# Performance work log

Measured on AMD Instinct MI355X. Metric: run time of the kernel, lower is better.

Reference implementation:

```python
import jax, jax.numpy as jnp
import numpy as np

D_IN, D_MODEL = 512, 256
B, N = 2, 512


def setup_inputs() -> dict:
    key = jax.random.key(0)
    ks = jax.random.split(key, 8)
    xav_x = float(np.sqrt(2.0 / (D_IN + D_MODEL)))
    xav_p = float(np.sqrt(2.0 / (4 + D_MODEL)))
    return {
        "x": jax.random.normal(ks[0], (B, N, D_IN), dtype=jnp.float32),
        "pos": jax.random.normal(ks[1], (B, N, 4), dtype=jnp.float32),
        "attn_mask": jax.random.randint(ks[2], (B, N, N), 0, 2, dtype=jnp.int32),
        "Wx": jax.random.normal(ks[3], (D_IN, D_MODEL), dtype=jnp.float32) * xav_x,
        "bx": jnp.zeros((D_MODEL,), dtype=jnp.float32),
        "Wp": jax.random.normal(ks[4], (4, D_MODEL), dtype=jnp.float32) * xav_p,
        "bp": jnp.zeros((D_MODEL,), dtype=jnp.float32),
        "w": jax.random.normal(ks[5], (D_MODEL,), dtype=jnp.float32) * 0.05,
    }


def reference(x, pos, attn_mask, Wx, bx, Wp, bp, w):
    # projected, activated inputs: [B, N, d_model]
    h = jnp.tanh(x @ Wx + bx)
    # pairwise relative positions: [B, N, N, 4]
    rel = pos[:, :, None, :] - pos[:, None, :, :]
    # position MLP + tanh: [B, N, N, d_model]
    z = jnp.tanh(rel @ Wp + bp)
    # scores via dot with weight vector: [B, N, N]
    attn = jnp.einsum("bijd,d->bij", z, w)
    mask = attn_mask != 0
    attn = jnp.where(mask, attn, -jnp.inf)
    attn = jax.nn.softmax(attn, axis=2)
    attn = jnp.where(mask, attn, 0.0)
    # dropout is identity in eval mode
    # weighted sum: [B, N, d_model]
    output = jnp.einsum("bij,bjd->bid", attn, h)
    return (output, attn)
```

## Files before the change

### kernel.cpp

```cpp
#include <hip/hip_runtime.h>
#include <hip/hip_bf16.h>
#include <math.h>

#define BATCH   2
#define SEQ     512
#define DIN     512
#define DM      256
#define DM4     (DM/4)

#define LOG2E2  2.88539008177792681f

#if __has_builtin(__builtin_amdgcn_exp2f)
#define EXP2(x) __builtin_amdgcn_exp2f(x)
#else
#define EXP2(x) exp2f(x)
#endif
#if __has_builtin(__builtin_amdgcn_rcpf)
#define RCP(x) __builtin_amdgcn_rcpf(x)
#else
#define RCP(x) (1.0f / (x))
#endif

__device__ __forceinline__ float tanh_from_scaled(float targ) {
    return fmaf(-2.0f, RCP(1.0f + EXP2(targ)), 1.0f);
}

__global__ __launch_bounds__(512) void produce_k(
    const float* __restrict__ pos,
    const float* __restrict__ Wp,
    const float* __restrict__ x,
    const float* __restrict__ Wx,
    const float* __restrict__ bx,
    float4* __restrict__ EB4,
    float* __restrict__ h)
{
    const int tid = threadIdx.x;
    const int idx = blockIdx.x;

    if (idx < 128) {
        const int b  = idx >> 6;
        const int d4 = idx & 63;
        const int d0 = 4 * d4;
        const float4 p = ((const float4*)pos)[b * SEQ + tid];
        float4 e;
        {
            const float P = fmaf(p.x, Wp[d0], fmaf(p.y, Wp[DM + d0],
                            fmaf(p.z, Wp[2*DM + d0], p.w * Wp[3*DM + d0])));
            e.x = EXP2(-LOG2E2 * P);
        }
        {
            const float P = fmaf(p.x, Wp[d0+1], fmaf(p.y, Wp[DM + d0+1],
                            fmaf(p.z, Wp[2*DM + d0+1], p.w * Wp[3*DM + d0+1])));
            e.y = EXP2(-LOG2E2 * P);
        }
        {
            const float P = fmaf(p.x, Wp[d0+2], fmaf(p.y, Wp[DM + d0+2],
                            fmaf(p.z, Wp[2*DM + d0+2], p.w * Wp[3*DM + d0+2])));
            e.z = EXP2(-LOG2E2 * P);
        }
        {
            const float P = fmaf(p.x, Wp[d0+3], fmaf(p.y, Wp[DM + d0+3],
                            fmaf(p.z, Wp[2*DM + d0+3], p.w * Wp[3*DM + d0+3])));
            e.w = EXP2(-LOG2E2 * P);
        }
        EB4[((size_t)(b * DM4 + d4)) * SEQ + tid] = e;
    }

    __shared__ float  s_xt[2][32][68];
    __shared__ float  s_wt[2][64][32];
    __shared__ float4 s_part[256];

    const int rt  = idx >> 3;
    const int ct  = idx & 7;
    const int kh  = __builtin_amdgcn_readfirstlane(tid >> 8);
    const int t   = tid & 255;
    const int ty  = t >> 3;
    const int tx  = t & 7;
    const int row = rt * 32 + ty;

    float4 acc = make_float4(0.f, 0.f, 0.f, 0.f);

    for (int ks = 0; ks < 4; ks++) {
        const int k0 = kh * 256 + ks * 64;
        #pragma unroll
        for (int s = 0; s < 2; s++) {
            const int fidx = t * 2 + s;
            const int r = fidx >> 4, c = fidx & 15;
            *(float4*)&s_xt[kh][r][4 * c] =
                *(const float4*)(x + (size_t)(rt * 32 + r) * DIN + k0 + 4 * c);
        }
        #pragma unroll
        for (int s = 0; s < 2; s++) {
            const int fidx = t * 2 + s;
            const int r = fidx >> 3, c = fidx & 7;
            *(float4*)&s_wt[kh][r][4 * c] =
                *(const float4*)(Wx + (size_t)(k0 + r) * DM + ct * 32 + 4 * c);
        }
        __syncthreads();

        #pragma unroll 8
        for (int k = 0; k < 64; k++) {
            const float  xv = s_xt[kh][ty][k];
            const float4 wq = *(const float4*)&s_wt[kh][k][4 * tx];
            acc.x = fmaf(xv, wq.x, acc.x);
            acc.y = fmaf(xv, wq.y, acc.y);
            acc.z = fmaf(xv, wq.z, acc.z);
            acc.w = fmaf(xv, wq.w, acc.w);
        }
        __syncthreads();
    }

    if (kh == 1) s_part[t] = acc;
    __syncthreads();
    if (kh == 0) {
        const float4 q4 = s_part[t];
        const float4 bq = *(const float4*)(bx + ct * 32 + 4 * tx);
        float4 o;
        o.x = tanh_from_scaled(LOG2E2 * (acc.x + q4.x + bq.x));
        o.y = tanh_from_scaled(LOG2E2 * (acc.y + q4.y + bq.y));
        o.z = tanh_from_scaled(LOG2E2 * (acc.z + q4.z + bq.z));
        o.w = tanh_from_scaled(LOG2E2 * (acc.w + q4.w + bq.w));
        *(float4*)(h + (size_t)row * DM + ct * 32 + 4 * tx) = o;
    }
}

__global__ __launch_bounds__(512) void attend_k(
    const float* __restrict__ pos,
    const float* __restrict__ Wp,
    const float* __restrict__ bp,
    const int*   __restrict__ mask,
    const float* __restrict__ wv,
    const float4* __restrict__ EB4,
    const float* __restrict__ h,
    float* __restrict__ out,
    float* __restrict__ attn_out)
{
    const int b   = blockIdx.x >> 7;
    const int i0  = (blockIdx.x & 127) * 4;
    const int tid = threadIdx.x;
    const int l   = tid & 63;

    __shared__ float4 s_ea[DM];
    __shared__ float  s_p[4][SEQ];
    __shared__ float  s_red[4][8];
    __shared__ float  s_o[7][4][DM];

    {
        const int d  = tid & 255;
        const int rp = __builtin_amdgcn_readfirstlane(tid >> 8);
        const int r0 = rp * 2;
        const float4 p0 = ((const float4*)pos)[b * SEQ + i0 + r0];
        const float4 p1 = ((const float4*)pos)[b * SEQ + i0 + r0 + 1];
        const float wp0 = Wp[d], wp1 = Wp[DM + d], wp2 = Wp[2*DM + d], wp3 = Wp[3*DM + d];
        const float bpd = bp[d];
        const float P0 = fmaf(p0.x, wp0, fmaf(p0.y, wp1, fmaf(p0.z, wp2, p0.w * wp3)));
        const float P1 = fmaf(p1.x, wp0, fmaf(p1.y, wp1, fmaf(p1.z, wp2, p1.w * wp3)));
        float* se = (float*)&s_ea[d];
        se[r0]     = EXP2(LOG2E2 * (P0 + bpd));
        se[r0 + 1] = EXP2(LOG2E2 * (P1 + bpd));
    }
    __syncthreads();

    const size_t mrow = (size_t)b * SEQ * SEQ + (size_t)i0 * SEQ + tid;
    const int m0 = mask[mrow];
    const int m1 = mask[mrow + SEQ];
    const int m2 = mask[mrow + 2*SEQ];
    const int m3 = mask[mrow + 3*SEQ];

    const float4* __restrict__ EBj = EB4 + (size_t)b * DM4 * SEQ + tid;

    float a0 = 0.f, a1 = 0.f, a2 = 0.f, a3 = 0.f;
    #pragma unroll 4
    for (int t = 0; t < DM4; t++) {
        const float4 eb = EBj[(size_t)t * SEQ];
        const float4 e0 = s_ea[4*t + 0];
        const float4 e1 = s_ea[4*t + 1];
        const float4 e2 = s_ea[4*t + 2];
        const float4 e3 = s_ea[4*t + 3];
        const float4 w4 = *(const float4*)(wv + 4*t);

#define SCORE_ROW(acc, C) { \
        const float y0 = fmaf(e0.C, eb.x, 1.f); \
        const float y1 = fmaf(e1.C, eb.y, 1.f); \
        const float y2 = fmaf(e2.C, eb.z, 1.f); \
        const float y3 = fmaf(e3.C, eb.w, 1.f); \
        acc = fmaf(fmaf(w4.x, y1, w4.y * y0), RCP(y0 * y1), acc); \
        acc = fmaf(fmaf(w4.z, y3, w4.w * y2), RCP(y2 * y3), acc); \
    }
        SCORE_ROW(a0, x)
        SCORE_ROW(a1, y)
        SCORE_ROW(a2, z)
        SCORE_ROW(a3, w)
#undef SCORE_ROW
    }

    float p0 = m0 ? EXP2(-LOG2E2 * a0) : 0.f;
    float p1 = m1 ? EXP2(-LOG2E2 * a1) : 0.f;
    float p2 = m2 ? EXP2(-LOG2E2 * a2) : 0.f;
    float p3 = m3 ? EXP2(-LOG2E2 * a3) : 0.f;

    float s0 = p0, s1 = p1, s2 = p2, s3 = p3;
    #pragma unroll
    for (int off = 32; off; off >>= 1) {
        s0 += __shfl_xor(s0, off, 64);
        s1 += __shfl_xor(s1, off, 64);
        s2 += __shfl_xor(s2, off, 64);
        s3 += __shfl_xor(s3, off, 64);
    }
    const int w = tid >> 6;
    if (l == 0) { s_red[0][w] = s0; s_red[1][w] = s1; s_red[2][w] = s2; s_red[3][w] = s3; }
    __syncthreads();

    {
        const float4 r0a = ((const float4*)s_red[0])[0], r0b = ((const float4*)s_red[0])[1];
        const float4 r1a = ((const float4*)s_red[1])[0], r1b = ((const float4*)s_red[1])[1];
        const float4 r2a = ((const float4*)s_red[2])[0], r2b = ((const float4*)s_red[2])[1];
        const float4 r3a = ((const float4*)s_red[3])[0], r3b = ((const float4*)s_red[3])[1];
        p0 *= __fdividef(1.0f, (r0a.x+r0a.y+r0a.z+r0a.w) + (r0b.x+r0b.y+r0b.z+r0b.w));
        p1 *= __fdividef(1.0f, (r1a.x+r1a.y+r1a.z+r1a.w) + (r1b.x+r1b.y+r1b.z+r1b.w));
        p2 *= __fdividef(1.0f, (r2a.x+r2a.y+r2a.z+r2a.w) + (r2b.x+r2b.y+r2b.z+r2b.w));
        p3 *= __fdividef(1.0f, (r3a.x+r3a.y+r3a.z+r3a.w) + (r3b.x+r3b.y+r3b.z+r3b.w));
    }

    attn_out[mrow]         = p0;
    attn_out[mrow + SEQ]   = p1;
    attn_out[mrow + 2*SEQ] = p2;
    attn_out[mrow + 3*SEQ] = p3;
    s_p[0][tid] = p0; s_p[1][tid] = p1; s_p[2][tid] = p2; s_p[3][tid] = p3;
    __syncthreads();

    const int dq = tid & 63;
    const int js = __builtin_amdgcn_readfirstlane(tid >> 6);
    const float* __restrict__ hp = h + (size_t)(b * SEQ + js * 64) * DM + 4 * dq;
    const float* __restrict__ q0p = &s_p[0][js * 64];
    const float* __restrict__ q1p = &s_p[1][js * 64];
    const float* __restrict__ q2p = &s_p[2][js * 64];
    const float* __restrict__ q3p = &s_p[3][js * 64];

    float4 a0v = make_float4(0,0,0,0), a1v = a0v, a2v = a0v, a3v = a0v;
    #pragma unroll 4
    for (int jj = 0; jj < 16; jj++) {
        const float4 P0 = *(const float4*)(q0p + 4 * jj);
        const float4 P1 = *(const float4*)(q1p + 4 * jj);
        const float4 P2 = *(const float4*)(q2p + 4 * jj);
        const float4 P3 = *(const float4*)(q3p + 4 * jj);
        const float4 h0 = *(const float4*)(hp + (size_t)(4*jj + 0) * DM);
        const float4 h1 = *(const float4*)(hp + (size_t)(4*jj + 1) * DM);
        const float4 h2 = *(const float4*)(hp + (size_t)(4*jj + 2) * DM);
        const float4 h3 = *(const float4*)(hp + (size_t)(4*jj + 3) * DM);

        a0v.x = fmaf(P0.x,h0.x,fmaf(P0.y,h1.x,fmaf(P0.z,h2.x,fmaf(P0.w,h3.x,a0v.x))));
        a0v.y = fmaf(P0.x,h0.y,fmaf(P0.y,h1.y,fmaf(P0.z,h2.y,fmaf(P0.w,h3.y,a0v.y))));
        a0v.z = fmaf(P0.x,h0.z,fmaf(P0.y,h1.z,fmaf(P0.z,h2.z,fmaf(P0.w,h3.z,a0v.z))));
        a0v.w = fmaf(P0.x,h0.w,fmaf(P0.y,h1.w,fmaf(P0.z,h2.w,fmaf(P0.w,h3.w,a0v.w))));
        a1v.x = fmaf(P1.x,h0.x,fmaf(P1.y,h1.x,fmaf(P1.z,h2.x,fmaf(P1.w,h3.x,a1v.x))));
        a1v.y = fmaf(P1.x,h0.y,fmaf(P1.y,h1.y,fmaf(P1.z,h2.y,fmaf(P1.w,h3.y,a1v.y))));
        a1v.z = fmaf(P1.x,h0.z,fmaf(P1.y,h1.z,fmaf(P1.z,h2.z,fmaf(P1.w,h3.z,a1v.z))));
        a1v.w = fmaf(P1.x,h0.w,fmaf(P1.y,h1.w,fmaf(P1.z,h2.w,fmaf(P1.w,h3.w,a1v.w))));
        a2v.x = fmaf(P2.x,h0.x,fmaf(P2.y,h1.x,fmaf(P2.z,h2.x,fmaf(P2.w,h3.x,a2v.x))));
        a2v.y = fmaf(P2.x,h0.y,fmaf(P2.y,h1.y,fmaf(P2.z,h2.y,fmaf(P2.w,h3.y,a2v.y))));
        a2v.z = fmaf(P2.x,h0.z,fmaf(P2.y,h1.z,fmaf(P2.z,h2.z,fmaf(P2.w,h3.z,a2v.z))));
        a2v.w = fmaf(P2.x,h0.w,fmaf(P2.y,h1.w,fmaf(P2.z,h2.w,fmaf(P2.w,h3.w,a2v.w))));
        a3v.x = fmaf(P3.x,h0.x,fmaf(P3.y,h1.x,fmaf(P3.z,h2.x,fmaf(P3.w,h3.x,a3v.x))));
        a3v.y = fmaf(P3.x,h0.y,fmaf(P3.y,h1.y,fmaf(P3.z,h2.y,fmaf(P3.w,h3.y,a3v.y))));
        a3v.z = fmaf(P3.x,h0.z,fmaf(P3.y,h1.z,fmaf(P3.z,h2.z,fmaf(P3.w,h3.z,a3v.z))));
        a3v.w = fmaf(P3.x,h0.w,fmaf(P3.y,h1.w,fmaf(P3.z,h2.w,fmaf(P3.w,h3.w,a3v.w))));
    }

    if (js > 0) {
        *(float4*)&s_o[js - 1][0][4 * dq] = a0v;
        *(float4*)&s_o[js - 1][1][4 * dq] = a1v;
        *(float4*)&s_o[js - 1][2][4 * dq] = a2v;
        *(float4*)&s_o[js - 1][3][4 * dq] = a3v;
    }
    __syncthreads();
    if (js == 0) {
        #pragma unroll
        for (int s = 0; s < 7; s++) {
            const float4 q0 = *(const float4*)&s_o[s][0][4 * dq];
            const float4 q1 = *(const float4*)&s_o[s][1][4 * dq];
            const float4 q2 = *(const float4*)&s_o[s][2][4 * dq];
            const float4 q3 = *(const float4*)&s_o[s][3][4 * dq];
            a0v.x += q0.x; a0v.y += q0.y; a0v.z += q0.z; a0v.w += q0.w;
            a1v.x += q1.x; a1v.y += q1.y; a1v.z += q1.z; a1v.w += q1.w;
            a2v.x += q2.x; a2v.y += q2.y; a2v.z += q2.z; a2v.w += q2.w;
            a3v.x += q3.x; a3v.y += q3.y; a3v.z += q3.z; a3v.w += q3.w;
        }
        float* __restrict__ op = out + (size_t)(b * SEQ + i0) * DM + 4 * dq;
        *(float4*)(op)        = a0v;
        *(float4*)(op + DM)   = a1v;
        *(float4*)(op + 2*DM) = a2v;
        *(float4*)(op + 3*DM) = a3v;
    }
}

extern "C" void kernel_launch(void* const* d_in, const int* in_sizes, int n_in,
                              void* d_out, int out_size, void* d_ws, size_t ws_size,
                              hipStream_t stream) {
    const float* x    = (const float*)d_in[0];
    const float* pos  = (const float*)d_in[1];
    const int*   mask = (const int*)  d_in[2];
    const float* Wx   = (const float*)d_in[3];
    const float* bx   = (const float*)d_in[4];
    const float* Wp   = (const float*)d_in[5];
    const float* bp   = (const float*)d_in[6];
    const float* wv   = (const float*)d_in[7];

    float* out      = (float*)d_out;
    float* attn_out = (float*)d_out + (size_t)BATCH*SEQ*DM;

    char*  ws  = (char*)d_ws;
    float* h   = (float*)(ws);
    float* EBf = (float*)(ws + (size_t)BATCH*SEQ*DM*4);

    produce_k<<<256, 512, 0, stream>>>(pos, Wp, x, Wx, bx, (float4*)EBf, h);
    attend_k <<<(BATCH*SEQ)/4, 512, 0, stream>>>(pos, Wp, bp, mask, wv,
                                                 (const float4*)EBf, h, out, attn_out);
}
```

Before: 99.15 us.

## Restructure h projection into 8-way split-K register tiles; merge score reciprocals

The x@Wx projection now stages the whole 512x32 Wx column slice in shared memory once, splits K across 8 wavefronts, and gives each thread a 4x4 register tile. x is read directly from global memory as float4, and the partials are reduced through shared memory. This replaces the two-stage loop with per-iteration syncs and raises FMA work per shared load. Separately, the score loop combines two rational terms so it needs one reciprocal per four dims instead of two. That cuts transcendental throughput but risks overflow or precision loss in the product of four y terms.

```diff
diff --git a/kernel.cpp b/kernel.cpp
--- a/kernel.cpp
+++ b/kernel.cpp
@@ -66,61 +66,74 @@
         EB4[((size_t)(b * DM4 + d4)) * SEQ + tid] = e;
     }
 
-    __shared__ float  s_xt[2][32][68];
-    __shared__ float  s_wt[2][64][32];
-    __shared__ float4 s_part[256];
-
-    const int rt  = idx >> 3;
-    const int ct  = idx & 7;
-    const int kh  = __builtin_amdgcn_readfirstlane(tid >> 8);
-    const int t   = tid & 255;
-    const int ty  = t >> 3;
-    const int tx  = t & 7;
-    const int row = rt * 32 + ty;
-
-    float4 acc = make_float4(0.f, 0.f, 0.f, 0.f);
-
-    for (int ks = 0; ks < 4; ks++) {
-        const int k0 = kh * 256 + ks * 64;
+    __shared__ float s_w[DIN][32];
+    __shared__ float s_part[8][32][36];
+
+    const int rt = idx >> 3;
+    const int ct = idx & 7;
+
+    #pragma unroll
+    for (int s = 0; s < 8; s++) {
+        const int q = tid + 512 * s;
+        const int k = q >> 3, c = q & 7;
+        *(float4*)&s_w[k][4 * c] =
+            *(const float4*)(Wx + (size_t)k * DM + ct * 32 + 4 * c);
+    }
+    __syncthreads();
+
+    const int ks = __builtin_amdgcn_readfirstlane(tid >> 6);
+    const int l  = tid & 63;
+    const int r4 = l >> 3;
+    const int c4 = l & 7;
+    const int k0 = ks * 64;
+
+    const float* __restrict__ xr = x + (size_t)(rt * 32 + 4 * r4) * DIN + k0;
+
+    float4 a0 = make_float4(0.f,0.f,0.f,0.f), a1 = a0, a2 = a0, a3 = a0;
+
+    #pragma unroll 4
+    for (int kk = 0; kk < 64; kk += 4) {
+        const float4 x0 = *(const float4*)(xr + kk);
+        const float4 x1 = *(const float4*)(xr + kk + DIN);
+        const float4 x2 = *(const float4*)(xr + kk + 2 * DIN);
+        const float4 x3 = *(const float4*)(xr + kk + 3 * DIN);
+#define GSTEP(C, J) { \
+        const float4 wq = *(const float4*)&s_w[k0 + kk + J][4 * c4]; \
+        a0.x = fmaf(x0.C, wq.x, a0.x); a0.y = fmaf(x0.C, wq.y, a0.y); \
+        a0.z = fmaf(x0.C, wq.z, a0.z); a0.w = fmaf(x0.C, wq.w, a0.w); \
+        a1.x = fmaf(x1.C, wq.x, a1.x); a1.y = fmaf(x1.C, wq.y, a1.y); \
+        a1.z = fmaf(x1.C, wq.z, a1.z); a1.w = fmaf(x1.C, wq.w, a1.w); \
+        a2.x = fmaf(x2.C, wq.x, a2.x); a2.y = fmaf(x2.C, wq.y, a2.y); \
+        a2.z = fmaf(x2.C, wq.z, a2.z); a2.w = fmaf(x2.C, wq.w, a2.w); \
+        a3.x = fmaf(x3.C, wq.x, a3.x); a3.y = fmaf(x3.C, wq.y, a3.y); \
+        a3.z = fmaf(x3.C, wq.z, a3.z); a3.w = fmaf(x3.C, wq.w, a3.w); \
+    }
+        GSTEP(x, 0) GSTEP(y, 1) GSTEP(z, 2) GSTEP(w, 3)
+#undef GSTEP
+    }
+
+    *(float4*)&s_part[ks][4 * r4 + 0][4 * c4] = a0;
+    *(float4*)&s_part[ks][4 * r4 + 1][4 * c4] = a1;
+    *(float4*)&s_part[ks][4 * r4 + 2][4 * c4] = a2;
+    *(float4*)&s_part[ks][4 * r4 + 3][4 * c4] = a3;
+    __syncthreads();
+
+    if (tid < 256) {
+        const int row = tid >> 3;
+        const int cq  = tid & 7;
+        float4 s = *(const float4*)&s_part[0][row][4 * cq];
         #pragma unroll
-        for (int s = 0; s < 2; s++) {
-            const int fidx = t * 2 + s;
-            const int r = fidx >> 4, c = fidx & 15;
-            *(float4*)&s_xt[kh][r][4 * c] =
-                *(const float4*)(x + (size_t)(rt * 32 + r) * DIN + k0 + 4 * c);
-        }
-        #pragma unroll
-        for (int s = 0; s < 2; s++) {
-            const int fidx = t * 2 + s;
-            const int r = fidx >> 3, c = fidx & 7;
-            *(float4*)&s_wt[kh][r][4 * c] =
-                *(const float4*)(Wx + (size_t)(k0 + r) * DM + ct * 32 + 4 * c);
-        }
-        __syncthreads();
-
-        #pragma unroll 8
-        for (int k = 0; k < 64; k++) {
-            const float  xv = s_xt[kh][ty][k];
-            const float4 wq = *(const float4*)&s_wt[kh][k][4 * tx];
-            acc.x = fmaf(xv, wq.x, acc.x);
-            acc.y = fmaf(xv, wq.y, acc.y);
-            acc.z = fmaf(xv, wq.z, acc.z);
-            acc.w = fmaf(xv, wq.w, acc.w);
-        }
-        __syncthreads();
-    }
-
-    if (kh == 1) s_part[t] = acc;
-    __syncthreads();
-    if (kh == 0) {
-        const float4 q4 = s_part[t];
-        const float4 bq = *(const float4*)(bx + ct * 32 + 4 * tx);
+        for (int p = 1; p < 8; p++) {
+            const float4 q = *(const float4*)&s_part[p][row][4 * cq];
+            s.x += q.x; s.y += q.y; s.z += q.z; s.w += q.w;
+        }
+        const float4 bq = *(const float4*)(bx + ct * 32 + 4 * cq);
         float4 o;
-        o.x = tanh_from_scaled(LOG2E2 * (acc.x + q4.x + bq.x));
-        o.y = tanh_from_scaled(LOG2E2 * (acc.y + q4.y + bq.y));
-        o.z = tanh_from_scaled(LOG2E2 * (acc.z + q4.z + bq.z));
-        o.w = tanh_from_scaled(LOG2E2 * (acc.w + q4.w + bq.w));
-        *(float4*)(h + (size_t)row * DM + ct * 32 + 4 * tx) = o;
+        o.x = tanh_from_scaled(LOG2E2 * (s.x + bq.x));
+        o.y = tanh_from_scaled(LOG2E2 * (s.y + bq.y));
+        o.z = tanh_from_scaled(LOG2E2 * (s.z + bq.z));
+        o.w = tanh_from_scaled(LOG2E2 * (s.w + bq.w));
+        *(float4*)(h + (size_t)(rt * 32 + row) * DM + ct * 32 + 4 * cq) = o;
     }
 }
 
@@ -184,8 +197,10 @@
         const float y1 = fmaf(e1.C, eb.y, 1.f); \
         const float y2 = fmaf(e2.C, eb.z, 1.f); \
         const float y3 = fmaf(e3.C, eb.w, 1.f); \
-        acc = fmaf(fmaf(w4.x, y1, w4.y * y0), RCP(y0 * y1), acc); \
-        acc = fmaf(fmaf(w4.z, y3, w4.w * y2), RCP(y2 * y3), acc); \
+        const float q01 = y0 * y1, q23 = y2 * y3; \
+        const float n01 = fmaf(w4.x, y1, w4.y * y0); \
+        const float n23 = fmaf(w4.z, y3, w4.w * y2); \
+        acc = fmaf(fmaf(n01, q23, n23 * q01), RCP(q01 * q23), acc); \
     }
         SCORE_ROW(a0, x)
         SCORE_ROW(a1, y)
```

New measurement: 95.74 us, median of 2. 3.4% less time.
